# Kernel tuning notes

Measured on AMD Instinct MI355X. Metric: run time of the kernel, lower is better.

Reference implementation:

```python
import jax, jax.numpy as jnp
import numpy as np

K = 2
CAPACITY_FACTOR = 1.25


def setup_inputs() -> dict:
    key = jax.random.key(0)
    ks = jax.random.split(key, 5)
    B, T, D, F, E = 4, 2048, 1024, 4096, 8
    x = jax.random.normal(ks[0], (B, T, D), dtype=jnp.float32)
    w_gate = jax.random.normal(ks[1], (E, D), dtype=jnp.float32) * (1.0 / np.sqrt(D))
    W1 = jax.random.normal(ks[2], (E, F, D), dtype=jnp.float32) * np.sqrt(2.0 / (D + F))
    b1 = jnp.zeros((E, F), dtype=jnp.float32)
    W2 = jax.random.normal(ks[3], (E, D, F), dtype=jnp.float32) * np.sqrt(2.0 / (D + F))
    b2 = jnp.zeros((E, D), dtype=jnp.float32)
    return {"x": x, "w_gate": w_gate, "W1": W1, "b1": b1, "W2": W2, "b2": b2}


def reference(x, w_gate, W1, b1, W2, b2):
    B, T, D = x.shape
    E = w_gate.shape[0]
    S = B * T
    C = int(CAPACITY_FACTOR * S * K / E)  # per-expert capacity
    tokens = x.reshape(S, D)

    # --- routing (fp32 softmax, top-k) ---
    logits = tokens @ w_gate.T                      # [S, E]
    probs = jax.nn.softmax(logits, axis=-1)         # [S, E]
    topk_vals, topk_idx = jax.lax.top_k(probs, K)   # [S, K]

    e_flat = topk_idx.reshape(-1)                   # [S*K] expert id per assignment
    g_flat = topk_vals.reshape(-1)                  # [S*K] gate value
    t_flat = jnp.repeat(jnp.arange(S), K)           # [S*K] source token index

    # --- capacity: position of each assignment within its expert (arrival order) ---
    onehot = jax.nn.one_hot(e_flat, E, dtype=jnp.int32)       # [S*K, E]
    pos = jnp.sum(jnp.cumsum(onehot, axis=0) * onehot, axis=-1) - 1  # [S*K]
    keep = pos < C

    # --- dispatch into [E, C, D] buffer (over-capacity assignments dropped) ---
    buf = jnp.zeros((E, C, D), dtype=tokens.dtype).at[e_flat, pos].set(
        tokens[t_flat], mode="drop")

    # --- grouped expert FFN: fc2(gelu(fc1(x))) + x  (exact gelu, as torch F.gelu) ---
    h = jax.nn.gelu(jnp.einsum("ecd,efd->ecf", buf, W1) + b1[:, None, :],
                    approximate=False)              # [E, C, F]
    expert_out = jnp.einsum("ecf,edf->ecd", h, W2) + b2[:, None, :] + buf  # [E, C, D]

    # --- combine: scatter-add gate-weighted expert outputs back to tokens ---
    gathered = expert_out[e_flat, jnp.clip(pos, 0, C - 1)]    # [S*K, D]
    w = jnp.where(keep, g_flat, 0.0)[:, None]
    y = jnp.zeros((S, D), dtype=tokens.dtype).at[t_flat].add(w * gathered)

    # --- load-balancing aux loss ---
    importance = probs.mean(axis=0)                            # [E]
    counts = jnp.zeros((E,), dtype=probs.dtype).at[e_flat].add(1.0)
    load = counts / S
    aux_loss = E * jnp.sum(importance * load)

    return y.reshape(B, T, D), aux_loss
```

## Files before the change

### kernel.cpp

```cpp
#include <hip/hip_runtime.h>
#include <hip/hip_bf16.h>
#include <math.h>
#include <stdint.h>

#define S_TOK 8192
#define D_DIM 1024
#define F_DIM 4096
#define E_EXP 8
#define C_CAP 2560

typedef __bf16 bf16x8_t __attribute__((ext_vector_type(8)));
typedef __bf16 bf16x4_t __attribute__((ext_vector_type(4)));
typedef float f32x4_t __attribute__((ext_vector_type(4)));

__device__ __forceinline__ void async_copy16(const void* g, void* l) {
  __builtin_amdgcn_global_load_lds(
      (const __attribute__((address_space(1))) unsigned int*)g,
      (__attribute__((address_space(3))) unsigned int*)l, 16, 0, 0);
}

__global__ __launch_bounds__(256) void routing_kernel(
    const float* __restrict__ x, const float* __restrict__ wg,
    __bf16* __restrict__ x_bf, int* __restrict__ asg_e, float* __restrict__ asg_g,
    float* __restrict__ imp_sum)
{
  __shared__ float s_imp[E_EXP];
  const int tid = threadIdx.x, lane = tid & 63, w = tid >> 6;
  if (tid < E_EXP) s_imp[tid] = 0.f;
  __syncthreads();
  const int t = blockIdx.x * 4 + w;

  const float4* xp = (const float4*)(x + (size_t)t * D_DIM);
  float4 xv[4];
#pragma unroll
  for (int j = 0; j < 4; j++) xv[j] = xp[lane + 64 * j];

#pragma unroll
  for (int j = 0; j < 4; j++) {
    bf16x4_t o;
    o[0] = (__bf16)xv[j].x; o[1] = (__bf16)xv[j].y;
    o[2] = (__bf16)xv[j].z; o[3] = (__bf16)xv[j].w;
    *(bf16x4_t*)(x_bf + (size_t)t * D_DIM + (size_t)(lane + 64 * j) * 4) = o;
  }

  float acc[E_EXP];
#pragma unroll
  for (int e = 0; e < E_EXP; e++) acc[e] = 0.f;
#pragma unroll
  for (int e = 0; e < E_EXP; e++) {
    const float4* wp = (const float4*)(wg + (size_t)e * D_DIM);
#pragma unroll
    for (int j = 0; j < 4; j++) {
      const float4 wv = wp[lane + 64 * j];
      acc[e] += xv[j].x * wv.x + xv[j].y * wv.y + xv[j].z * wv.z + xv[j].w * wv.w;
    }
  }
#pragma unroll
  for (int e = 0; e < E_EXP; e++)
    for (int off = 32; off > 0; off >>= 1) acc[e] += __shfl_xor(acc[e], off);

  if (lane == 0) {
    float m = acc[0];
#pragma unroll
    for (int e = 1; e < E_EXP; e++) m = fmaxf(m, acc[e]);
    float p[E_EXP], s = 0.f;
#pragma unroll
    for (int e = 0; e < E_EXP; e++) { p[e] = expf(acc[e] - m); s += p[e]; }
    const float inv = 1.f / s;
#pragma unroll
    for (int e = 0; e < E_EXP; e++) p[e] *= inv;
    int e0 = 0; float v0 = p[0];
#pragma unroll
    for (int e = 1; e < E_EXP; e++) if (p[e] > v0) { v0 = p[e]; e0 = e; }
    int e1 = -1; float v1 = -1.f;
#pragma unroll
    for (int e = 0; e < E_EXP; e++) if (e != e0 && p[e] > v1) { v1 = p[e]; e1 = e; }
    asg_e[2 * t] = e0; asg_g[2 * t] = v0;
    asg_e[2 * t + 1] = e1; asg_g[2 * t + 1] = v1;
#pragma unroll
    for (int e = 0; e < E_EXP; e++) atomicAdd(&s_imp[e], p[e]);
  }
  __syncthreads();
  if (tid < E_EXP) atomicAdd(&imp_sum[tid], s_imp[tid]);
}

__global__ __launch_bounds__(256) void cvt_kernel(const float* __restrict__ src,
                                                  __bf16* __restrict__ dst, int n4)
{
  const int stride = gridDim.x * blockDim.x;
  for (int i = blockIdx.x * blockDim.x + threadIdx.x; i < n4; i += stride) {
    const float4 v = ((const float4*)src)[i];
    bf16x4_t o;
    o[0] = (__bf16)v.x; o[1] = (__bf16)v.y; o[2] = (__bf16)v.z; o[3] = (__bf16)v.w;
    ((bf16x4_t*)dst)[i] = o;
  }
}

__global__ __launch_bounds__(256) void positions_kernel(
    const int* __restrict__ asg_e, const float* __restrict__ asg_g,
    const float* __restrict__ imp_sum, int* __restrict__ slot_token,
    float* __restrict__ slot_gate, int* __restrict__ cnt_g, float* __restrict__ aux_out)
{
  __shared__ int lcnt[E_EXP * 256];
  __shared__ int tot[E_EXP];
  const int tid = threadIdx.x;
  for (int i = tid; i < E_EXP * C_CAP; i += 256) slot_token[i] = -1;
  int cnt[E_EXP];
#pragma unroll
  for (int e = 0; e < E_EXP; e++) cnt[e] = 0;
  const int a0 = tid * 64;
  for (int j = 0; j < 64; j++) cnt[asg_e[a0 + j]]++;
#pragma unroll
  for (int e = 0; e < E_EXP; e++) lcnt[e * 256 + tid] = cnt[e];
  __syncthreads();
  if (tid < E_EXP) {
    int run = 0;
    for (int i = 0; i < 256; i++) { const int v = lcnt[tid * 256 + i]; lcnt[tid * 256 + i] = run; run += v; }
    tot[tid] = run;
    cnt_g[tid] = run;
  }
  __syncthreads();
  int base[E_EXP];
#pragma unroll
  for (int e = 0; e < E_EXP; e++) base[e] = lcnt[e * 256 + tid];
  for (int j = 0; j < 64; j++) {
    const int a = a0 + j;
    const int e = asg_e[a];
    const int pp = base[e]++;
    if (pp < C_CAP) { slot_token[e * C_CAP + pp] = a >> 1; slot_gate[e * C_CAP + pp] = asg_g[a]; }
  }
  if (tid == 0) {
    float aux = 0.f;
#pragma unroll
    for (int e = 0; e < E_EXP; e++) aux += imp_sum[e] * (float)tot[e];
    aux_out[0] = (float)E_EXP * aux / ((float)S_TOK * (float)S_TOK);
  }
}

template <int MODE>
__global__ __launch_bounds__(256, 3) void moe_gemm(
    const __bf16* __restrict__ A, const __bf16* __restrict__ Bw,
    const float* __restrict__ bias, const int* __restrict__ slot_token,
    const float* __restrict__ slot_gate, const float* __restrict__ xres,
    const int* __restrict__ cnt, __bf16* __restrict__ Hout, float* __restrict__ y,
    int MT, int NT, int N, int K)
{
  const int ntiles = gridDim.x;
  const int xcd = blockIdx.x & 7, slot = blockIdx.x >> 3;
  const int tile = xcd * (ntiles >> 3) + slot;
  const int e = tile / (MT * NT);
  const int t = tile % (MT * NT);
  const int grp = t / (4 * NT), rem = t % (4 * NT);
  const int mt = grp * 4 + (rem & 3), nt = rem >> 2;
  const int m0 = mt * 128, n0 = nt * 128;
  if (m0 >= cnt[e]) return;

  const int tid = threadIdx.x, lane = tid & 63, w = tid >> 6;
  const int wm = w >> 1, wn = w & 1;

  __shared__ __align__(16) unsigned short sA[128 * 64];
  __shared__ __align__(16) unsigned short sB[128 * 64];

  const int rstage = lane >> 3;
  const int cstage = (lane & 7) ^ rstage;

  const char* gA[4];
  const char* gB[4];
  void* lA[4];
  void* lB[4];
#pragma unroll
  for (int i = 0; i < 4; i++) {
    const int rowA = w * 32 + i * 8 + rstage;
    size_t arow;
    if (MODE == 0) {
      int tok = slot_token[e * C_CAP + m0 + rowA];
      if (tok < 0) tok = 0;
      arow = (size_t)tok * (size_t)K;
    } else {
      arow = ((size_t)(e * C_CAP + m0 + rowA)) * (size_t)K;
    }
    gA[i] = (const char*)(A + arow) + cstage * 16;
    lA[i] = (void*)&sA[(w * 32 + i * 8) * 64];
    const int rowB = w * 32 + i * 8 + rstage;
    const size_t brow = ((size_t)(e * N + n0 + rowB)) * (size_t)K;
    gB[i] = (const char*)(Bw + brow) + cstage * 16;
    lB[i] = (void*)&sB[(w * 32 + i * 8) * 64];
  }

  f32x4_t acc[4][4];
#pragma unroll
  for (int mi = 0; mi < 4; mi++)
#pragma unroll
    for (int ni = 0; ni < 4; ni++) acc[mi][ni] = (f32x4_t){0.f, 0.f, 0.f, 0.f};

  const int fr = lane & 15;
  const int fq = lane >> 4;
  for (int k0 = 0; k0 < K; k0 += 64) {
    const size_t koff = (size_t)k0 * 2;
    __syncthreads();
#pragma unroll
    for (int i = 0; i < 4; i++) async_copy16(gA[i] + koff, lA[i]);
#pragma unroll
    for (int i = 0; i < 4; i++) async_copy16(gB[i] + koff, lB[i]);
    __syncthreads();
#pragma unroll
    for (int kk = 0; kk < 2; kk++) {
      bf16x8_t af[4], bfv[4];
#pragma unroll
      for (int mi = 0; mi < 4; mi++) {
        const int row = wm * 64 + mi * 16 + fr;
        const int chk = (kk * 4 + fq) ^ (row & 7);
        af[mi] = *(const bf16x8_t*)&sA[row * 64 + chk * 8];
      }
#pragma unroll
      for (int ni = 0; ni < 4; ni++) {
        const int row = wn * 64 + ni * 16 + fr;
        const int chk = (kk * 4 + fq) ^ (row & 7);
        bfv[ni] = *(const bf16x8_t*)&sB[row * 64 + chk * 8];
      }
#pragma unroll
      for (int mi = 0; mi < 4; mi++)
#pragma unroll
        for (int ni = 0; ni < 4; ni++)
          acc[mi][ni] = __builtin_amdgcn_mfma_f32_16x16x32_bf16(af[mi], bfv[ni], acc[mi][ni], 0, 0, 0);
    }
  }

  const int col_lo = lane & 15;
  const int row_hi = (lane >> 4) * 4;
  if (MODE == 0) {
#pragma unroll
    for (int ni = 0; ni < 4; ni++) {
      const int gcol = n0 + wn * 64 + ni * 16 + col_lo;
      const float bv = bias[e * N + gcol];
#pragma unroll
      for (int mi = 0; mi < 4; mi++) {
#pragma unroll
        for (int r = 0; r < 4; r++) {
          const int grow = m0 + wm * 64 + mi * 16 + row_hi + r;
          const float v = acc[mi][ni][r] + bv;
          const float gl = 0.5f * v * (1.0f + erff(v * 0.70710678118654752f));
          Hout[((size_t)(e * C_CAP + grow)) * (size_t)N + gcol] = (__bf16)gl;
        }
      }
    }
  } else {
#pragma unroll
    for (int mi = 0; mi < 4; mi++) {
#pragma unroll
      for (int r = 0; r < 4; r++) {
        const int slot = e * C_CAP + m0 + wm * 64 + mi * 16 + row_hi + r;
        const int tok = slot_token[slot];
        if (tok < 0) continue;
        const float g = slot_gate[slot];
        const size_t trow = (size_t)tok * (size_t)N;
#pragma unroll
        for (int ni = 0; ni < 4; ni++) {
          const int gcol = n0 + wn * 64 + ni * 16 + col_lo;
          const float v = acc[mi][ni][r] + bias[e * N + gcol] + xres[trow + gcol];
          atomicAdd(&y[trow + gcol], g * v);
        }
      }
    }
  }
}

extern "C" void kernel_launch(void* const* d_in, const int* in_sizes, int n_in,
                              void* d_out, int out_size, void* d_ws, size_t ws_size,
                              hipStream_t stream) {
  const float* x  = (const float*)d_in[0];
  const float* wg = (const float*)d_in[1];
  const float* W1 = (const float*)d_in[2];
  const float* b1 = (const float*)d_in[3];
  const float* W2 = (const float*)d_in[4];
  const float* b2 = (const float*)d_in[5];
  float* y = (float*)d_out;

  char* p = (char*)d_ws;
  __bf16* x_bf = (__bf16*)p;    p += (size_t)S_TOK * D_DIM * 2;
  __bf16* w1_bf = (__bf16*)p;   p += (size_t)E_EXP * F_DIM * D_DIM * 2;
  __bf16* w2_bf = (__bf16*)p;   p += (size_t)E_EXP * F_DIM * D_DIM * 2;
  __bf16* Hbuf = (__bf16*)p;    p += (size_t)E_EXP * C_CAP * F_DIM * 2;
  int* slot_token = (int*)p;    p += (size_t)E_EXP * C_CAP * 4;
  float* slot_gate = (float*)p; p += (size_t)E_EXP * C_CAP * 4;
  int* asg_e = (int*)p;         p += (size_t)S_TOK * 2 * 4;
  float* asg_g = (float*)p;     p += (size_t)S_TOK * 2 * 4;
  float* imp_sum = (float*)p;   p += 64;
  int* cnt_g = (int*)p;         p += 64;

  hipMemsetAsync(d_out, 0, ((size_t)S_TOK * D_DIM + 1) * sizeof(float), stream);
  hipMemsetAsync(imp_sum, 0, E_EXP * sizeof(float), stream);

  routing_kernel<<<S_TOK / 4, 256, 0, stream>>>(x, wg, x_bf, asg_e, asg_g, imp_sum);
  cvt_kernel<<<2048, 256, 0, stream>>>(W1, w1_bf, E_EXP * F_DIM * D_DIM / 4);
  cvt_kernel<<<2048, 256, 0, stream>>>(W2, w2_bf, E_EXP * F_DIM * D_DIM / 4);
  positions_kernel<<<1, 256, 0, stream>>>(asg_e, asg_g, imp_sum, slot_token, slot_gate,
                                          cnt_g, y + (size_t)S_TOK * D_DIM);
  moe_gemm<0><<<E_EXP * 20 * 32, 256, 0, stream>>>(x_bf, w1_bf, b1, slot_token, nullptr, nullptr,
                                                   cnt_g, Hbuf, nullptr, 20, 32, F_DIM, D_DIM);
  moe_gemm<1><<<E_EXP * 20 * 8, 256, 0, stream>>>(Hbuf, w2_bf, b2, slot_token, slot_gate, x,
                                                  cnt_g, nullptr, y, 20, 8, D_DIM, F_DIM);
}
```

Baseline: 883.6 us.

## Double-buffer LDS tiles in MoE GEMM and use tanh-form GELU

The GEMM main loop now uses two 32-wide K-slices of LDS. The next slice is prefetched with async global-to-LDS copies while MFMAs run on the current one, which cuts the loop to one barrier per iteration and overlaps loads with compute. The swizzle is adjusted for the narrower 32-element rows. The fc1 epilogue also replaces the exact erf GELU with the tanh approximation written as a sigmoid, which is cheaper but departs slightly from the exact GELU the reference uses. The smaller K step doubles the iteration count and barriers per unit of work.

```diff
diff --git a/kernel.cpp b/kernel.cpp
--- a/kernel.cpp
+++ b/kernel.cpp
@@ -146,8 +146,8 @@
     int MT, int NT, int N, int K)
 {
   const int ntiles = gridDim.x;
-  const int xcd = blockIdx.x & 7, slot = blockIdx.x >> 3;
-  const int tile = xcd * (ntiles >> 3) + slot;
+  const int xcd = blockIdx.x & 7, bslot = blockIdx.x >> 3;
+  const int tile = xcd * (ntiles >> 3) + bslot;
   const int e = tile / (MT * NT);
   const int t = tile % (MT * NT);
   const int grp = t / (4 * NT), rem = t % (4 * NT);
@@ -158,19 +158,20 @@
   const int tid = threadIdx.x, lane = tid & 63, w = tid >> 6;
   const int wm = w >> 1, wn = w & 1;
 
-  __shared__ __align__(16) unsigned short sA[128 * 64];
-  __shared__ __align__(16) unsigned short sB[128 * 64];
-
-  const int rstage = lane >> 3;
-  const int cstage = (lane & 7) ^ rstage;
-
-  const char* gA[4];
-  const char* gB[4];
-  void* lA[4];
-  void* lB[4];
-#pragma unroll
-  for (int i = 0; i < 4; i++) {
-    const int rowA = w * 32 + i * 8 + rstage;
+  __shared__ __align__(16) unsigned short sA[2][128 * 32];
+  __shared__ __align__(16) unsigned short sB[2][128 * 32];
+
+  const int rs = lane >> 2;
+  const int cs = lane & 3;
+  const int csrc = cs ^ ((rs >> 1) & 3);
+
+  const char* gA[2];
+  const char* gB[2];
+  unsigned short* lA[2];
+  unsigned short* lB[2];
+#pragma unroll
+  for (int i = 0; i < 2; i++) {
+    const int rowA = w * 32 + i * 16 + rs;
     size_t arow;
     if (MODE == 0) {
       int tok = slot_token[e * C_CAP + m0 + rowA];
@@ -179,12 +180,12 @@
     } else {
       arow = ((size_t)(e * C_CAP + m0 + rowA)) * (size_t)K;
     }
-    gA[i] = (const char*)(A + arow) + cstage * 16;
-    lA[i] = (void*)&sA[(w * 32 + i * 8) * 64];
-    const int rowB = w * 32 + i * 8 + rstage;
+    gA[i] = (const char*)(A + arow) + csrc * 16;
+    lA[i] = &sA[0][(w * 32 + i * 16) * 32];
+    const int rowB = w * 32 + i * 16 + rs;
     const size_t brow = ((size_t)(e * N + n0 + rowB)) * (size_t)K;
-    gB[i] = (const char*)(Bw + brow) + cstage * 16;
-    lB[i] = (void*)&sB[(w * 32 + i * 8) * 64];
+    gB[i] = (const char*)(Bw + brow) + csrc * 16;
+    lB[i] = &sB[0][(w * 32 + i * 16) * 32];
   }
 
   f32x4_t acc[4][4];
@@ -193,37 +194,42 @@
 #pragma unroll
     for (int ni = 0; ni < 4; ni++) acc[mi][ni] = (f32x4_t){0.f, 0.f, 0.f, 0.f};
 
+  const int NIT = K >> 5;
+#pragma unroll
+  for (int i = 0; i < 2; i++) { async_copy16(gA[i], lA[i]); async_copy16(gB[i], lB[i]); }
+
   const int fr = lane & 15;
-  const int fq = lane >> 4;
-  for (int k0 = 0; k0 < K; k0 += 64) {
-    const size_t koff = (size_t)k0 * 2;
+  const int fkey = (fr >> 1) & 3;
+  const int quad = lane >> 4;
+
+  for (int it = 0; it < NIT; ++it) {
+    const int cur = it & 1;
     __syncthreads();
-#pragma unroll
-    for (int i = 0; i < 4; i++) async_copy16(gA[i] + koff, lA[i]);
-#pragma unroll
-    for (int i = 0; i < 4; i++) async_copy16(gB[i] + koff, lB[i]);
-    __syncthreads();
-#pragma unroll
-    for (int kk = 0; kk < 2; kk++) {
-      bf16x8_t af[4], bfv[4];
-#pragma unroll
-      for (int mi = 0; mi < 4; mi++) {
-        const int row = wm * 64 + mi * 16 + fr;
-        const int chk = (kk * 4 + fq) ^ (row & 7);
-        af[mi] = *(const bf16x8_t*)&sA[row * 64 + chk * 8];
+    if (it + 1 < NIT) {
+      const size_t koff = (size_t)(it + 1) * 64;
+      const int nxt = (cur ^ 1) * (128 * 32);
+#pragma unroll
+      for (int i = 0; i < 2; i++) {
+        async_copy16(gA[i] + koff, lA[i] + nxt);
+        async_copy16(gB[i] + koff, lB[i] + nxt);
       }
-#pragma unroll
-      for (int ni = 0; ni < 4; ni++) {
-        const int row = wn * 64 + ni * 16 + fr;
-        const int chk = (kk * 4 + fq) ^ (row & 7);
-        bfv[ni] = *(const bf16x8_t*)&sB[row * 64 + chk * 8];
-      }
-#pragma unroll
-      for (int mi = 0; mi < 4; mi++)
-#pragma unroll
-        for (int ni = 0; ni < 4; ni++)
-          acc[mi][ni] = __builtin_amdgcn_mfma_f32_16x16x32_bf16(af[mi], bfv[ni], acc[mi][ni], 0, 0, 0);
-    }
+    }
+    bf16x8_t af[4], bfv[4];
+#pragma unroll
+    for (int mi = 0; mi < 4; mi++) {
+      const int row = wm * 64 + mi * 16 + fr;
+      af[mi] = *(const bf16x8_t*)&sA[cur][row * 32 + (quad ^ fkey) * 8];
+    }
+#pragma unroll
+    for (int ni = 0; ni < 4; ni++) {
+      const int row = wn * 64 + ni * 16 + fr;
+      bfv[ni] = *(const bf16x8_t*)&sB[cur][row * 32 + (quad ^ fkey) * 8];
+    }
+#pragma unroll
+    for (int mi = 0; mi < 4; mi++)
+#pragma unroll
+      for (int ni = 0; ni < 4; ni++)
+        acc[mi][ni] = __builtin_amdgcn_mfma_f32_16x16x32_bf16(af[mi], bfv[ni], acc[mi][ni], 0, 0, 0);
   }
 
   const int col_lo = lane & 15;
@@ -239,7 +245,8 @@
         for (int r = 0; r < 4; r++) {
           const int grow = m0 + wm * 64 + mi * 16 + row_hi + r;
           const float v = acc[mi][ni][r] + bv;
-          const float gl = 0.5f * v * (1.0f + erff(v * 0.70710678118654752f));
+          const float z2 = 1.5957691216057308f * (v + 0.044715f * v * v * v);
+          const float gl = v / (1.f + __expf(-z2));
           Hout[((size_t)(e * C_CAP + grow)) * (size_t)N + gcol] = (__bf16)gl;
         }
       }
```

Measured after the change: 949.1 us. 1.07x slower.
